# Performance work log

Measured on AMD Instinct MI355X. Metric: run time of the kernel, lower is better.

Reference implementation:

```python
import jax, jax.numpy as jnp
import numpy as np

B, S, VOCAB, HID, NH, L, SPAN = 4, 512, 25, 512, 8, 12, 512
HEAD = HID // NH
FF = 4 * HID
EPS = 1e-7  # DebertaV2 layer_norm_eps


def _ln(x, g, b):
    m = x.mean(-1, keepdims=True)
    v = ((x - m) ** 2).mean(-1, keepdims=True)
    return (x - m) / jnp.sqrt(v + EPS) * g + b


def setup_inputs() -> dict:
    key = jax.random.key(0)
    ks = iter(jax.random.split(key, 16))
    w = lambda shape: jax.random.normal(next(ks), shape, jnp.float32) * 0.05
    return {
        "x": jax.random.randint(next(ks), (B, S), 0, VOCAB),
        "attention_mask": jnp.ones((B, S), jnp.int32),
        "word_emb": w((VOCAB, HID)),
        "emb_ln_g": jnp.ones((HID,), jnp.float32),
        "emb_ln_b": jnp.zeros((HID,), jnp.float32),
        "rel_emb": w((2 * SPAN, HID)),
        "Wq": w((L, HID, HID)), "bq": jnp.zeros((L, HID), jnp.float32),
        "Wk": w((L, HID, HID)), "bk": jnp.zeros((L, HID), jnp.float32),
        "Wv": w((L, HID, HID)), "bv": jnp.zeros((L, HID), jnp.float32),
        "Wpk": w((L, HID, HID)), "bpk": jnp.zeros((L, HID), jnp.float32),
        "Wpq": w((L, HID, HID)), "bpq": jnp.zeros((L, HID), jnp.float32),
        "Wo": w((L, HID, HID)), "bo": jnp.zeros((L, HID), jnp.float32),
        "ln1_g": jnp.ones((L, HID), jnp.float32), "ln1_b": jnp.zeros((L, HID), jnp.float32),
        "W1": w((L, HID, FF)), "b1": jnp.zeros((L, FF), jnp.float32),
        "W2": w((L, FF, HID)), "b2": jnp.zeros((L, HID), jnp.float32),
        "ln2_g": jnp.ones((L, HID), jnp.float32), "ln2_b": jnp.zeros((L, HID), jnp.float32),
        "cls_w": w((VOCAB, HID)), "cls_b": jnp.zeros((VOCAB,), jnp.float32),
    }


def _forward(x, attention_mask, word_emb, emb_ln_g, emb_ln_b, rel_emb,
             Wq, bq, Wk, bk, Wv, bv, Wpk, bpk, Wpq, bpq, Wo, bo,
             ln1_g, ln1_b, W1, b1, W2, b2, ln2_g, ln2_b, cls_w, cls_b):
    mask = attention_mask.astype(jnp.float32)
    # embeddings: word only (position_biased_input=False), LN, then masked
    h = _ln(word_emb[x], emb_ln_g, emb_ln_b) * mask[..., None]

    rel = jnp.arange(S)[:, None] - jnp.arange(S)[None, :]          # q_pos - k_pos
    c2p_idx = jnp.clip(rel + SPAN, 0, 2 * SPAN - 1)[None, None]    # [1,1,S,S]
    p2c_idx = jnp.clip(-rel + SPAN, 0, 2 * SPAN - 1)[None, None]
    attm = (mask[:, None, None, :] * mask[:, None, :, None]) > 0   # [B,1,S,S]
    scale = jnp.sqrt(jnp.float32(HEAD * 3))                        # scale_factor = 1 + len(pos_att_type)
    neg = jnp.finfo(jnp.float32).min

    def heads(t):  # [B,S,HID] -> [B,NH,S,HEAD]
        return t.reshape(B, S, NH, HEAD).transpose(0, 2, 1, 3)

    for l in range(L):
        q = heads(h @ Wq[l] + bq[l])
        k = heads(h @ Wk[l] + bk[l])
        v = heads(h @ Wv[l] + bv[l])
        # projected relative-position embeddings: [NH, 2*SPAN, HEAD]
        pk = (rel_emb @ Wpk[l] + bpk[l]).reshape(2 * SPAN, NH, HEAD).transpose(1, 0, 2)
        pq = (rel_emb @ Wpq[l] + bpq[l]).reshape(2 * SPAN, NH, HEAD).transpose(1, 0, 2)

        scores = jnp.einsum('bhqd,bhkd->bhqk', q, k)
        # c2p: query content vs key position, gathered at clamp(rel+span)
        c2p = jnp.take_along_axis(jnp.einsum('bhqd,hpd->bhqp', q, pk), c2p_idx, axis=-1)
        # p2c: key content vs query position, gathered at clamp(-rel+span) then transposed
        p2c = jnp.take_along_axis(jnp.einsum('bhkd,hpd->bhkp', k, pq), p2c_idx, axis=-1)
        scores = (scores + c2p + jnp.swapaxes(p2c, -1, -2)) / scale

        scores = jnp.where(attm, scores, neg)
        probs = jnp.where(attm, jax.nn.softmax(scores, axis=-1), 0.0)  # XSoftmax
        ctx = jnp.einsum('bhqk,bhkd->bhqd', probs, v).transpose(0, 2, 1, 3).reshape(B, S, HID)
        h = _ln(ctx @ Wo[l] + bo[l] + h, ln1_g[l], ln1_b[l])
        f = jax.nn.gelu(h @ W1[l] + b1[l], approximate=False) @ W2[l] + b2[l]
        h = _ln(f + h, ln2_g[l], ln2_b[l])

    logits = h @ cls_w.T + cls_b
    return h, logits


def reference(x, attention_mask, word_emb, emb_ln_g, emb_ln_b, rel_emb,
              Wq, bq, Wk, bk, Wv, bv, Wpk, bpk, Wpq, bpq, Wo, bo,
              ln1_g, ln1_b, W1, b1, W2, b2, ln2_g, ln2_b, cls_w, cls_b):
    return _forward(x, attention_mask, word_emb, emb_ln_g, emb_ln_b, rel_emb,
                    Wq, bq, Wk, bk, Wv, bv, Wpk, bpk, Wpq, bpq, Wo, bo,
                    ln1_g, ln1_b, W1, b1, W2, b2, ln2_g, ln2_b, cls_w, cls_b)
```

## Files before the change

kernel.cpp:

```cpp
#include <hip/hip_runtime.h>
#include <hip/hip_bf16.h>

#define BATCH  4
#define SEQ    512
#define TOK    (BATCH*SEQ)
#define HID    512
#define NHEAD  8
#define HEAD   64
#define FFDIM  2048
#define NLAYER 12
#define SPAN2  1024
#define VOCAB  25
#define LNEPS  1e-7f
#define NEG_BIG -3.0e38f

typedef __attribute__((ext_vector_type(8))) short bf16x8;
typedef __attribute__((ext_vector_type(4))) float floatx4;

#define MFMA16(a, b, c) __builtin_amdgcn_mfma_f32_16x16x32_bf16((a), (b), (c), 0, 0, 0)

__device__ __forceinline__ float b2f(unsigned short u) {
    return __uint_as_float(((unsigned int)u) << 16);
}
__device__ __forceinline__ unsigned short f2b(float f) {
    __hip_bfloat16 h = __float2bfloat16(f);
    return *(unsigned short*)&h;
}

__device__ __forceinline__ float block_reduce_sum(float v, float* red) {
    int tid = threadIdx.x;
    red[tid] = v; __syncthreads();
    for (int s = 128; s > 0; s >>= 1) { if (tid < s) red[tid] += red[tid + s]; __syncthreads(); }
    float r = red[0]; __syncthreads();
    return r;
}

__global__ void embed_ln_kernel(const int* __restrict__ x, const int* __restrict__ am,
                                const float* __restrict__ word_emb,
                                const float* __restrict__ g, const float* __restrict__ bb,
                                float* __restrict__ h, unsigned short* __restrict__ hb) {
    __shared__ float red[256];
    int t = blockIdx.x, tid = threadIdx.x;
    const float* we = word_emb + (size_t)x[t] * HID;
    float v1 = we[tid], v2 = we[tid + 256];
    float mean = block_reduce_sum(v1 + v2, red) * (1.0f / HID);
    float d1 = v1 - mean, d2 = v2 - mean;
    float var = block_reduce_sum(d1 * d1 + d2 * d2, red) * (1.0f / HID);
    float rstd = rsqrtf(var + LNEPS);
    float maskf = (float)am[t];
    size_t base = (size_t)t * HID;
    float o1 = (d1 * rstd * g[tid]       + bb[tid])       * maskf;
    float o2 = (d2 * rstd * g[tid + 256] + bb[tid + 256]) * maskf;
    h[base + tid] = o1;        h[base + tid + 256] = o2;
    hb[base + tid] = f2b(o1);  hb[base + tid + 256] = f2b(o2);
}

__global__ void add_ln_kernel(const float* __restrict__ tmp,
                              const float* __restrict__ g, const float* __restrict__ bb,
                              float* __restrict__ h, unsigned short* __restrict__ hb) {
    __shared__ float red[256];
    int t = blockIdx.x, tid = threadIdx.x;
    size_t base = (size_t)t * HID;
    float v1 = tmp[base + tid] + h[base + tid];
    float v2 = tmp[base + tid + 256] + h[base + tid + 256];
    float mean = block_reduce_sum(v1 + v2, red) * (1.0f / HID);
    float d1 = v1 - mean, d2 = v2 - mean;
    float var = block_reduce_sum(d1 * d1 + d2 * d2, red) * (1.0f / HID);
    float rstd = rsqrtf(var + LNEPS);
    float o1 = d1 * rstd * g[tid]       + bb[tid];
    float o2 = d2 * rstd * g[tid + 256] + bb[tid + 256];
    h[base + tid] = o1;        h[base + tid + 256] = o2;
    hb[base + tid] = f2b(o1);  hb[base + tid + 256] = f2b(o2);
}

__global__ void add_ln2_kernel(const float* __restrict__ t1a, const float* __restrict__ t1b,
                               const float* __restrict__ g, const float* __restrict__ bb,
                               float* __restrict__ h, unsigned short* __restrict__ hb) {
    __shared__ float red[256];
    int t = blockIdx.x, tid = threadIdx.x;
    size_t base = (size_t)t * HID;
    float v1 = t1a[base + tid] + t1b[base + tid] + h[base + tid];
    float v2 = t1a[base + tid + 256] + t1b[base + tid + 256] + h[base + tid + 256];
    float mean = block_reduce_sum(v1 + v2, red) * (1.0f / HID);
    float d1 = v1 - mean, d2 = v2 - mean;
    float var = block_reduce_sum(d1 * d1 + d2 * d2, red) * (1.0f / HID);
    float rstd = rsqrtf(var + LNEPS);
    float o1 = d1 * rstd * g[tid]       + bb[tid];
    float o2 = d2 * rstd * g[tid + 256] + bb[tid + 256];
    h[base + tid] = o1;        h[base + tid + 256] = o2;
    hb[base + tid] = f2b(o1);  hb[base + tid + 256] = f2b(o2);
}

__global__ void cvt_rel_kernel(const float* __restrict__ in, unsigned short* __restrict__ out) {
    int i = (blockIdx.x * 256 + threadIdx.x) * 4;
    float4 v = *(const float4*)(in + i);
    out[i] = f2b(v.x); out[i+1] = f2b(v.y); out[i+2] = f2b(v.z); out[i+3] = f2b(v.w);
}

__global__ void tcvt_kernel(const float* __restrict__ in, unsigned short* __restrict__ out,
                            int K, int N) {
    __shared__ float tile[32][33];
    int l = blockIdx.z;
    const float* ip = in + (size_t)l * K * N;
    unsigned short* op = out + (size_t)l * K * N;
    int kb = blockIdx.y * 32, nb = blockIdx.x * 32;
    int tx = threadIdx.x, ty = threadIdx.y;
    #pragma unroll
    for (int i = 0; i < 32; i += 8) tile[ty + i][tx] = ip[(size_t)(kb + ty + i) * N + nb + tx];
    __syncthreads();
    #pragma unroll
    for (int i = 0; i < 32; i += 8) op[(size_t)(nb + ty + i) * K + kb + tx] = f2b(tile[tx][ty + i]);
}

__global__ void tcvt6_kernel(const float* __restrict__ Wq, const float* __restrict__ Wk,
                             const float* __restrict__ Wv, const float* __restrict__ Wpk,
                             const float* __restrict__ Wpq, const float* __restrict__ Wo,
                             unsigned short* __restrict__ out) {
    __shared__ float tile[32][33];
    int z = blockIdx.z, l = z / 6, w = z - l * 6;
    const float* src = w == 0 ? Wq : w == 1 ? Wk : w == 2 ? Wv : w == 3 ? Wpk : w == 4 ? Wpq : Wo;
    const float* ip = src + (size_t)l * HID * HID;
    unsigned short* op = out + ((size_t)w * NLAYER + l) * HID * HID;
    int kb = blockIdx.y * 32, nb = blockIdx.x * 32;
    int tx = threadIdx.x, ty = threadIdx.y;
    #pragma unroll
    for (int i = 0; i < 32; i += 8) tile[ty + i][tx] = ip[(size_t)(kb + ty + i) * HID + nb + tx];
    __syncthreads();
    #pragma unroll
    for (int i = 0; i < 32; i += 8) op[(size_t)(nb + ty + i) * HID + kb + tx] = f2b(tile[tx][ty + i]);
}

__device__ __forceinline__ void gemm_tile_bt(
    const unsigned short* __restrict__ A, const unsigned short* __restrict__ Bt,
    int row0, int col0, int K, int kbeg, int kend,
    floatx4 (&acc)[2][2], unsigned short (&As)[2][64][72], unsigned short (&Bs)[2][64][72]) {
    int tid = threadIdx.x;
    int lane = tid & 63, wid = tid >> 6;
    int wm = wid >> 1, wn = wid & 1;
    int m16 = lane & 15, quad = lane >> 4;
    int sr = tid >> 2, sc = (tid & 3) << 4;
    const unsigned short* Ag = A + (size_t)(row0 + sr) * K + sc;
    const unsigned short* Bg = Bt + (size_t)(col0 + sr) * K + sc;

    uint4 av0 = *(const uint4*)(Ag + kbeg);
    uint4 av1 = *(const uint4*)(Ag + kbeg + 8);
    uint4 bv0 = *(const uint4*)(Bg + kbeg);
    uint4 bv1 = *(const uint4*)(Bg + kbeg + 8);
    *(uint4*)&As[0][sr][sc]     = av0;
    *(uint4*)&As[0][sr][sc + 8] = av1;
    *(uint4*)&Bs[0][sr][sc]     = bv0;
    *(uint4*)&Bs[0][sr][sc + 8] = bv1;
    __syncthreads();

    int cur = 0;
    for (int k0 = kbeg; k0 < kend; k0 += 64) {
        int k1 = k0 + 64;
        bool more = k1 < kend;
        if (more) {
            av0 = *(const uint4*)(Ag + k1);
            av1 = *(const uint4*)(Ag + k1 + 8);
            bv0 = *(const uint4*)(Bg + k1);
            bv1 = *(const uint4*)(Bg + k1 + 8);
        }
        #pragma unroll
        for (int kk = 0; kk < 2; kk++) {
            bf16x8 a0 = *(const bf16x8*)&As[cur][wm * 32 + m16][kk * 32 + quad * 8];
            bf16x8 a1 = *(const bf16x8*)&As[cur][wm * 32 + 16 + m16][kk * 32 + quad * 8];
            bf16x8 b0 = *(const bf16x8*)&Bs[cur][wn * 32 + m16][kk * 32 + quad * 8];
            bf16x8 b1 = *(const bf16x8*)&Bs[cur][wn * 32 + 16 + m16][kk * 32 + quad * 8];
            acc[0][0] = MFMA16(a0, b0, acc[0][0]);
            acc[0][1] = MFMA16(a0, b1, acc[0][1]);
            acc[1][0] = MFMA16(a1, b0, acc[1][0]);
            acc[1][1] = MFMA16(a1, b1, acc[1][1]);
        }
        if (more) {
            *(uint4*)&As[cur ^ 1][sr][sc]     = av0;
            *(uint4*)&As[cur ^ 1][sr][sc + 8] = av1;
            *(uint4*)&Bs[cur ^ 1][sr][sc]     = bv0;
            *(uint4*)&Bs[cur ^ 1][sr][sc + 8] = bv1;
            __syncthreads();
            cur ^= 1;
        }
    }
}

template<bool OUT_BF16, bool GELU, int SPLITK>
__global__ __launch_bounds__(256) void gemm_bt(
    const unsigned short* __restrict__ A, const unsigned short* __restrict__ Bt,
    const float* __restrict__ bias, void* __restrict__ Cp, int N, int K) {
    __shared__ unsigned short As[2][64][72], Bs[2][64][72];
    int row0 = blockIdx.y * 64, col0 = blockIdx.x * 64;
    int kseg = K / SPLITK;
    int kbeg = kseg * blockIdx.z, kend = kbeg + kseg;
    floatx4 acc[2][2];
    #pragma unroll
    for (int mi = 0; mi < 2; mi++)
        #pragma unroll
        for (int ni = 0; ni < 2; ni++) acc[mi][ni] = (floatx4){0.f, 0.f, 0.f, 0.f};
    gemm_tile_bt(A, Bt, row0, col0, K, kbeg, kend, acc, As, Bs);

    int tid = threadIdx.x, lane = tid & 63, wid = tid >> 6;
    int wm = wid >> 1, wn = wid & 1, m16 = lane & 15, quad = lane >> 4;
    size_t outoff = (size_t)blockIdx.z * (size_t)(gridDim.y << 6) * N;
    #pragma unroll
    for (int ni = 0; ni < 2; ni++) {
        int colg = col0 + wn * 32 + ni * 16 + m16;
        float bval = (SPLITK == 1 || blockIdx.z == 0) ? bias[colg] : 0.0f;
        #pragma unroll
        for (int mi = 0; mi < 2; mi++) {
            #pragma unroll
            for (int r = 0; r < 4; r++) {
                int rowg = row0 + wm * 32 + mi * 16 + quad * 4 + r;
                float v = acc[mi][ni][r] + bval;
                if (GELU) v = 0.5f * v * (1.0f + erff(v * 0.70710678118654752f));
                if (OUT_BF16) ((unsigned short*)Cp)[(size_t)rowg * N + colg] = f2b(v);
                else          ((float*)Cp)[outoff + (size_t)rowg * N + colg] = v;
            }
        }
    }
}

__global__ __launch_bounds__(256) void qkvp_gemm(
    const unsigned short* __restrict__ hb, const unsigned short* __restrict__ relb,
    const unsigned short* __restrict__ Wqt, const unsigned short* __restrict__ Wkt,
    const unsigned short* __restrict__ Wvt, const unsigned short* __restrict__ Wpkt,
    const unsigned short* __restrict__ Wpqt,
    const float* __restrict__ bq, const float* __restrict__ bk, const float* __restrict__ bv,
    const float* __restrict__ bpk, const float* __restrict__ bpq,
    unsigned short* __restrict__ qb, unsigned short* __restrict__ kb,
    unsigned short* __restrict__ vb, unsigned short* __restrict__ pkb,
    unsigned short* __restrict__ pqb) {
    __shared__ unsigned short As[2][64][72], Bs[2][64][72];
    int bid = blockIdx.x;
    int xcd = bid & 7, slot = bid >> 3;
    int op, j;
    if (xcd < 6) { op = xcd >> 1; j = slot * 2 + (xcd & 1); }
    else         { op = xcd - 3;  j = slot; }
    int trow = j >> 3, tcol = j & 7;
    const unsigned short* A; const unsigned short* Bt; const float* bias; unsigned short* C;
    if (op < 3) {
        A = hb;
        Bt   = op == 0 ? Wqt : op == 1 ? Wkt : Wvt;
        bias = op == 0 ? bq  : op == 1 ? bk  : bv;
        C    = op == 0 ? qb  : op == 1 ? kb  : vb;
    } else {
        A = relb;
        Bt   = op == 3 ? Wpkt : Wpqt;
        bias = op == 3 ? bpk  : bpq;
        C    = op == 3 ? pkb  : pqb;
    }
    floatx4 acc[2][2];
    #pragma unroll
    for (int mi = 0; mi < 2; mi++)
        #pragma unroll
        for (int ni = 0; ni < 2; ni++) acc[mi][ni] = (floatx4){0.f, 0.f, 0.f, 0.f};
    gemm_tile_bt(A, Bt, trow * 64, tcol * 64, HID, 0, HID, acc, As, Bs);

    int tid = threadIdx.x, lane = tid & 63, wid = tid >> 6;
    int wm = wid >> 1, wn = wid & 1, m16 = lane & 15, quad = lane >> 4;
    #pragma unroll
    for (int ni = 0; ni < 2; ni++) {
        int colg = tcol * 64 + wn * 32 + ni * 16 + m16;
        float bval = bias[colg];
        #pragma unroll
        for (int mi = 0; mi < 2; mi++) {
            #pragma unroll
            for (int r = 0; r < 4; r++) {
                int rowg = trow * 64 + wm * 32 + mi * 16 + quad * 4 + r;
                C[(size_t)rowg * HID + colg] = f2b(acc[mi][ni][r] + bval);
            }
        }
    }
}

template<bool OUT_BF16, bool GELU>
__global__ __launch_bounds__(256) void mfma_gemm(
    const unsigned short* __restrict__ A, const float* __restrict__ B,
    const float* __restrict__ bias, void* __restrict__ Cp, int N, int K) {
    __shared__ unsigned short As[64][72];
    __shared__ unsigned short Bs[64][72];
    int tid = threadIdx.x;
    int lane = tid & 63, wid = tid >> 6;
    int wm = wid >> 1, wn = wid & 1;
    int row0 = blockIdx.y * 64, col0 = blockIdx.x * 64;
    int m16 = lane & 15, quad = lane >> 4;

    int ar = tid >> 2, ac = (tid & 3) << 4;
    int bk = (tid >> 3) << 1, bn = (tid & 7) << 3;

    const unsigned short* Ag = A + (size_t)(row0 + ar) * K + ac;
    const float* Bg = B + (size_t)bk * N + col0 + bn;

    floatx4 acc[2][2];
    #pragma unroll
    for (int mi = 0; mi < 2; mi++)
        #pragma unroll
        for (int ni = 0; ni < 2; ni++) acc[mi][ni] = (floatx4){0.f, 0.f, 0.f, 0.f};

    for (int k0 = 0; k0 < K; k0 += 64) {
        uint4 av0 = *(const uint4*)(Ag + k0);
        uint4 av1 = *(const uint4*)(Ag + k0 + 8);
        const float* br0 = Bg + (size_t)k0 * N;
        const float* br1 = br0 + N;
        float4 b00 = *(const float4*)br0, b01 = *(const float4*)(br0 + 4);
        float4 b10 = *(const float4*)br1, b11 = *(const float4*)(br1 + 4);
        *(uint4*)&As[ar][ac] = av0;
        *(uint4*)&As[ar][ac + 8] = av1;
        float lo[8] = {b00.x, b00.y, b00.z, b00.w, b01.x, b01.y, b01.z, b01.w};
        float hi[8] = {b10.x, b10.y, b10.z, b10.w, b11.x, b11.y, b11.z, b11.w};
        #pragma unroll
        for (int i = 0; i < 8; i++) {
            unsigned int p = (unsigned int)f2b(lo[i]) | ((unsigned int)f2b(hi[i]) << 16);
            *(unsigned int*)&Bs[bn + i][bk] = p;
        }
        __syncthreads();
        #pragma unroll
        for (int kk = 0; kk < 2; kk++) {
            bf16x8 a0 = *(const bf16x8*)&As[wm * 32 + m16][kk * 32 + quad * 8];
            bf16x8 a1 = *(const bf16x8*)&As[wm * 32 + 16 + m16][kk * 32 + quad * 8];
            bf16x8 b0 = *(const bf16x8*)&Bs[wn * 32 + m16][kk * 32 + quad * 8];
            bf16x8 b1 = *(const bf16x8*)&Bs[wn * 32 + 16 + m16][kk * 32 + quad * 8];
            acc[0][0] = MFMA16(a0, b0, acc[0][0]);
            acc[0][1] = MFMA16(a0, b1, acc[0][1]);
            acc[1][0] = MFMA16(a1, b0, acc[1][0]);
            acc[1][1] = MFMA16(a1, b1, acc[1][1]);
        }
        __syncthreads();
    }
    #pragma unroll
    for (int ni = 0; ni < 2; ni++) {
        int colg = col0 + wn * 32 + ni * 16 + m16;
        float bv = bias[colg];
        #pragma unroll
        for (int mi = 0; mi < 2; mi++) {
            #pragma unroll
            for (int r = 0; r < 4; r++) {
                int rowg = row0 + wm * 32 + mi * 16 + quad * 4 + r;
                float v = acc[mi][ni][r] + bv;
                if (GELU) v = 0.5f * v * (1.0f + erff(v * 0.70710678118654752f));
                if (OUT_BF16) ((unsigned short*)Cp)[(size_t)rowg * N + colg] = f2b(v);
                else          ((float*)Cp)[(size_t)rowg * N + colg] = v;
            }
        }
    }
}

__global__ __launch_bounds__(256, 2) void attn_kernel(
    const unsigned short* __restrict__ Q, const unsigned short* __restrict__ K,
    const unsigned short* __restrict__ V,
    const unsigned short* __restrict__ PK, const unsigned short* __restrict__ PQ,
    const int* __restrict__ am, unsigned short* __restrict__ ctx) {
    __shared__ unsigned short Ks[2][32][72];
    __shared__ unsigned short Vt[2][64][40];
    __shared__ float Afs[4][16][49];
    __shared__ float Bfs[4][32][50];
    __shared__ unsigned short Pls[4][16][40];
    __shared__ int mkk[2][32];
    __shared__ float mergeML[2][2][16];

    int bid = blockIdx.x;
    int hh = bid & 7;
    int b  = (bid >> 3) & 3;
    int q0 = (bid >> 5) * 32;
    int tid = threadIdx.x;
    int lane = tid & 63, wave = tid >> 6;
    int u = wave >> 1;
    int s = wave & 1;
    int quad = lane >> 4, m16 = lane & 15;
    const float inv_scale = 0.07216878364870323f;

    const unsigned short* qg = Q + (size_t)(b * SEQ + q0 + u * 16 + m16) * HID + hh * HEAD;
    bf16x8 qf0 = *(const bf16x8*)(qg + quad * 8);
    bf16x8 qf1 = *(const bf16x8*)(qg + 32 + quad * 8);

    int sr = tid >> 3;
    int sc = (tid & 7) * 8;
    int vkey = ((sc >> 3) & 3) << 3;

    floatx4 accO[4];
    #pragma unroll
    for (int nt = 0; nt < 4; nt++) accO[nt] = (floatx4){0.f, 0.f, 0.f, 0.f};
    float mreg[4] = {NEG_BIG, NEG_BIG, NEG_BIG, NEG_BIG};
    float lreg[4] = {0.f, 0.f, 0.f, 0.f};

    for (int ph = 0; ph < 8; ph++) {
        int t = 2 * ph + s;
        int P0  = q0 - 32 * t + 481;
        int P20 = 32 * t - q0 + 481;
        int Jb  = 16 - 16 * u;

        bf16x8 pkf[3][2], pqf[3][2];
        #pragma unroll
        for (int nt = 0; nt < 3; nt++) {
            int prow = P0 + 16 * u + nt * 16 + m16;
            const unsigned short* pg = PK + (size_t)prow * HID + hh * HEAD + quad * 8;
            pkf[nt][0] = *(const bf16x8*)pg;
            pkf[nt][1] = *(const bf16x8*)(pg + 32);
            int prow2 = P20 + Jb + nt * 16 + m16;
            if (prow2 > 1023) prow2 = 1023;
            const unsigned short* pg2 = PQ + (size_t)prow2 * HID + hh * HEAD + quad * 8;
            pqf[nt][0] = *(const bf16x8*)pg2;
            pqf[nt][1] = *(const bf16x8*)(pg2 + 32);
        }

        #pragma unroll
        for (int sl = 0; sl < 2; sl++) {
            int k0 = ph * 64 + sl * 32;
            const unsigned short* kg = K + (size_t)(b * SEQ + k0 + sr) * HID + hh * HEAD + sc;
            *(uint4*)&Ks[sl][sr][sc] = *(const uint4*)kg;
            uint4 vv = *(const uint4*)(V + (size_t)(b * SEQ + k0 + sr) * HID + hh * HEAD + sc);
            unsigned short* vp = (unsigned short*)&vv;
            #pragma unroll
            for (int j = 0; j < 8; j++) Vt[sl][sc + j][sr ^ vkey] = vp[j];
        }
        if (tid < 64) mkk[tid >> 5][tid & 31] = am[b * SEQ + ph * 64 + tid];
        __syncthreads();

        floatx4 accS[2];
        accS[0] = (floatx4){0.f, 0.f, 0.f, 0.f};
        accS[1] = (floatx4){0.f, 0.f, 0.f, 0.f};
        #pragma unroll
        for (int n = 0; n < 2; n++) {
            bf16x8 kfa = *(const bf16x8*)&Ks[s][n * 16 + m16][quad * 8];
            bf16x8 kfb = *(const bf16x8*)&Ks[s][n * 16 + m16][32 + quad * 8];
            accS[n] = MFMA16(qf0, kfa, accS[n]);
            accS[n] = MFMA16(qf1, kfb, accS[n]);
        }

        {
            floatx4 accA[3];
            #pragma unroll
            for (int nt = 0; nt < 3; nt++) {
                accA[nt] = (floatx4){0.f, 0.f, 0.f, 0.f};
                accA[nt] = MFMA16(qf0, pkf[nt][0], accA[nt]);
                accA[nt] = MFMA16(qf1, pkf[nt][1], accA[nt]);
            }
            #pragma unroll
            for (int nt = 0; nt < 3; nt++)
                #pragma unroll
                for (int r = 0; r < 4; r++)
                    Afs[wave][quad * 4 + r][nt * 16 + m16] = accA[nt][r];
        }

        {
            floatx4 accB[2][3];
            #pragma unroll
            for (int mt = 0; mt < 2; mt++) {
                bf16x8 afa = *(const bf16x8*)&Ks[s][mt * 16 + m16][quad * 8];
                bf16x8 afb = *(const bf16x8*)&Ks[s][mt * 16 + m16][32 + quad * 8];
                #pragma unroll
                for (int nt = 0; nt < 3; nt++) {
                    accB[mt][nt] = (floatx4){0.f, 0.f, 0.f, 0.f};
                    accB[mt][nt] = MFMA16(afa, pqf[nt][0], accB[mt][nt]);
                    accB[mt][nt] = MFMA16(afb, pqf[nt][1], accB[mt][nt]);
                }
            }
            #pragma unroll
            for (int mt = 0; mt < 2; mt++)
                #pragma unroll
                for (int nt = 0; nt < 3; nt++)
                    #pragma unroll
                    for (int r = 0; r < 4; r++)
                        Bfs[wave][mt * 16 + quad * 4 + r][nt * 16 + m16] = accB[mt][nt][r];
        }

        float sv[2][4];
        float tmax[4] = {NEG_BIG, NEG_BIG, NEG_BIG, NEG_BIG};
        #pragma unroll
        for (int n = 0; n < 2; n++) {
            #pragma unroll
            for (int r = 0; r < 4; r++) {
                int qq = quad * 4 + r;
                int kc = n * 16 + m16;
                float av = Afs[wave][qq][qq - kc + 31];
                float bv = Bfs[wave][kc][kc - qq + 15];
                float x = (accS[n][r] + av + bv) * inv_scale;
                x = mkk[s][kc] ? x : NEG_BIG;
                sv[n][r] = x;
                tmax[r] = fmaxf(tmax[r], x);
            }
        }
        float alpha[4], psum[4];
        #pragma unroll
        for (int r = 0; r < 4; r++) {
            float tm = tmax[r];
            tm = fmaxf(tm, __shfl_xor(tm, 1));
            tm = fmaxf(tm, __shfl_xor(tm, 2));
            tm = fmaxf(tm, __shfl_xor(tm, 4));
            tm = fmaxf(tm, __shfl_xor(tm, 8));
            float mo = mreg[r];
            float mn = fmaxf(mo, tm);
            alpha[r] = __expf(mo - mn);
            mreg[r] = mn;
        }
        #pragma unroll
        for (int r = 0; r < 4; r++) psum[r] = 0.f;
        #pragma unroll
        for (int n = 0; n < 2; n++) {
            #pragma unroll
            for (int r = 0; r < 4; r++) {
                float p = (sv[n][r] > -1.5e38f) ? __expf(sv[n][r] - mreg[r]) : 0.0f;
                unsigned short pb = f2b(p);
                Pls[wave][quad * 4 + r][n * 16 + m16] = pb;
                psum[r] += b2f(pb);
            }
        }
        #pragma unroll
        for (int r = 0; r < 4; r++) {
            float ps = psum[r];
            ps += __shfl_xor(ps, 1);
            ps += __shfl_xor(ps, 2);
            ps += __shfl_xor(ps, 4);
            ps += __shfl_xor(ps, 8);
            lreg[r] = lreg[r] * alpha[r] + ps;
        }
        #pragma unroll
        for (int nt = 0; nt < 4; nt++)
            #pragma unroll
            for (int r = 0; r < 4; r++) accO[nt][r] *= alpha[r];
        {
            bf16x8 pf = *(const bf16x8*)&Pls[wave][m16][quad * 8];
            #pragma unroll
            for (int nt = 0; nt < 4; nt++) {
                int d = nt * 16 + m16;
                int kq = (quad ^ ((d >> 3) & 3)) * 8;
                bf16x8 vf = *(const bf16x8*)&Vt[s][d][kq];
                accO[nt] = MFMA16(pf, vf, accO[nt]);
            }
        }
        __syncthreads();
    }

    __syncthreads();
    float* mo = &Bfs[0][0][0];
    if (s == 1) {
        #pragma unroll
        for (int nt = 0; nt < 4; nt++)
            #pragma unroll
            for (int r = 0; r < 4; r++)
                mo[u * 1056 + (quad * 4 + r) * 66 + nt * 16 + m16] = accO[nt][r];
        if (m16 == 0) {
            #pragma unroll
            for (int r = 0; r < 4; r++) {
                mergeML[u][0][quad * 4 + r] = mreg[r];
                mergeML[u][1][quad * 4 + r] = lreg[r];
            }
        }
    }
    __syncthreads();
    if (s == 0) {
        #pragma unroll
        for (int r = 0; r < 4; r++) {
            int row = quad * 4 + r;
            float m1 = mergeML[u][0][row], l1 = mergeML[u][1][row];
            float m0 = mreg[r], l0 = lreg[r];
            float mt = fmaxf(m0, m1);
            float a0 = __expf(m0 - mt), a1 = __expf(m1 - mt);
            float lt = l0 * a0 + l1 * a1;
            float inv = lt > 0.0f ? 1.0f / lt : 0.0f;
            inv *= (float)am[b * SEQ + q0 + u * 16 + row];
            #pragma unroll
            for (int nt = 0; nt < 4; nt++) {
                float o1 = mo[u * 1056 + row * 66 + nt * 16 + m16];
                float val = (accO[nt][r] * a0 + o1 * a1) * inv;
                ctx[(size_t)(b * SEQ + q0 + u * 16 + row) * HID + hh * HEAD + nt * 16 + m16] = f2b(val);
            }
        }
    }
}

__global__ void copy_f_kernel(const float* __restrict__ in, float* __restrict__ out, int n) {
    int i = blockIdx.x * 256 + threadIdx.x;
    if (i < n) out[i] = in[i];
}
__global__ void cls_kernel(const float* __restrict__ h, const float* __restrict__ cls_w,
                           const float* __restrict__ cls_b, float* __restrict__ out) {
    int t = blockIdx.x, v = threadIdx.x;
    if (v < VOCAB) {
        const float* hr = h + (size_t)t * HID;
        const float* wr = cls_w + (size_t)v * HID;
        float acc = cls_b[v];
        for (int d = 0; d < HID; d++) acc += hr[d] * wr[d];
        out[t * VOCAB + v] = acc;
    }
}

extern "C" void kernel_launch(void* const* d_in, const int* in_sizes, int n_in,
                              void* d_out, int out_size, void* d_ws, size_t ws_size,
                              hipStream_t stream) {
    const int* x     = (const int*)d_in[0];
    const int* am    = (const int*)d_in[1];
    const float* word_emb = (const float*)d_in[2];
    const float* emb_g    = (const float*)d_in[3];
    const float* emb_b    = (const float*)d_in[4];
    const float* rel_emb  = (const float*)d_in[5];
    const float* Wq  = (const float*)d_in[6];  const float* bq  = (const float*)d_in[7];
    const float* Wk  = (const float*)d_in[8];  const float* bk  = (const float*)d_in[9];
    const float* Wv  = (const float*)d_in[10]; const float* bv  = (const float*)d_in[11];
    const float* Wpk = (const float*)d_in[12]; const float* bpk = (const float*)d_in[13];
    const float* Wpq = (const float*)d_in[14]; const float* bpq = (const float*)d_in[15];
    const float* Wo  = (const float*)d_in[16]; const float* bo  = (const float*)d_in[17];
    const float* ln1g = (const float*)d_in[18]; const float* ln1b = (const float*)d_in[19];
    const float* W1  = (const float*)d_in[20]; const float* b1  = (const float*)d_in[21];
    const float* W2  = (const float*)d_in[22]; const float* b2  = (const float*)d_in[23];
    const float* ln2g = (const float*)d_in[24]; const float* ln2b = (const float*)d_in[25];
    const float* cls_w = (const float*)d_in[26]; const float* cls_b = (const float*)d_in[27];

    char* wsb = (char*)d_ws;
    const size_t NEED_BIG = 107u << 20;

    if (ws_size >= NEED_BIG) {
        float* h  = (float*)wsb;
        float* t1 = (float*)(wsb + (4u << 20));
        float* t2 = (float*)(wsb + (8u << 20));
        unsigned short* qb   = (unsigned short*)(wsb + (12u << 20));
        unsigned short* kb   = (unsigned short*)(wsb + (14u << 20));
        unsigned short* vb   = (unsigned short*)(wsb + (16u << 20));
        unsigned short* pkb  = (unsigned short*)(wsb + (18u << 20));
        unsigned short* pqb  = (unsigned short*)(wsb + (19u << 20));
        unsigned short* relb = (unsigned short*)(wsb + (20u << 20));
        unsigned short* hb   = (unsigned short*)(wsb + (21u << 20));
        unsigned short* ctx  = hb;
        unsigned short* ffb  = qb;
        unsigned short* Wqt  = (unsigned short*)(wsb + (23u << 20));
        unsigned short* W1t  = (unsigned short*)(wsb + (59u << 20));
        unsigned short* W2t  = (unsigned short*)(wsb + (83u << 20));

        const size_t M512 = (size_t)HID * HID;

        tcvt6_kernel<<<dim3(16, 16, 72), dim3(32, 8), 0, stream>>>(Wq, Wk, Wv, Wpk, Wpq, Wo, Wqt);
        tcvt_kernel<<<dim3(64, 16, 12), dim3(32, 8), 0, stream>>>(W1, W1t, HID, FFDIM);
        tcvt_kernel<<<dim3(16, 64, 12), dim3(32, 8), 0, stream>>>(W2, W2t, FFDIM, HID);
        cvt_rel_kernel<<<dim3(SPAN2 * HID / 1024), dim3(256), 0, stream>>>(rel_emb, relb);
        embed_ln_kernel<<<dim3(TOK), dim3(256), 0, stream>>>(x, am, word_emb, emb_g, emb_b, h, hb);

        for (int l = 0; l < NLAYER; l++) {
            qkvp_gemm<<<dim3(1024), dim3(256), 0, stream>>>(
                hb, relb,
                Wqt + (size_t)(0 * NLAYER + l) * M512, Wqt + (size_t)(1 * NLAYER + l) * M512,
                Wqt + (size_t)(2 * NLAYER + l) * M512, Wqt + (size_t)(3 * NLAYER + l) * M512,
                Wqt + (size_t)(4 * NLAYER + l) * M512,
                bq + l * HID, bk + l * HID, bv + l * HID, bpk + l * HID, bpq + l * HID,
                qb, kb, vb, pkb, pqb);

            attn_kernel<<<dim3(512), dim3(256), 0, stream>>>(
                qb, kb, vb, pkb, pqb, am, ctx);

            gemm_bt<false, false, 2><<<dim3(HID / 64, TOK / 64, 2), dim3(256), 0, stream>>>(
                ctx, Wqt + (size_t)(5 * NLAYER + l) * M512, bo + l * HID, t1, HID, HID);
            add_ln2_kernel<<<dim3(TOK), dim3(256), 0, stream>>>(t1, t2, ln1g + l * HID, ln1b + l * HID, h, hb);

            gemm_bt<true, true, 1><<<dim3(FFDIM / 64, TOK / 64, 1), dim3(256), 0, stream>>>(
                hb, W1t + (size_t)l * HID * FFDIM, b1 + l * FFDIM, ffb, FFDIM, HID);
            gemm_bt<false, false, 2><<<dim3(HID / 64, TOK / 64, 2), dim3(256), 0, stream>>>(
                ffb, W2t + (size_t)l * HID * FFDIM, b2 + l * HID, t1, HID, FFDIM);
            add_ln2_kernel<<<dim3(TOK), dim3(256), 0, stream>>>(t1, t2, ln2g + l * HID, ln2b + l * HID, h, hb);
        }

        float* out_f = (float*)d_out;
        copy_f_kernel<<<dim3(TOK * HID / 256), dim3(256), 0, stream>>>(h, out_f, TOK * HID);
        cls_kernel<<<dim3(TOK), dim3(32), 0, stream>>>(h, cls_w, cls_b, out_f + TOK * HID);
        return;
    }

    const size_t NEEDED = 19u << 20;
    if (ws_size < NEEDED) return;
    float* h  = (float*)wsb;
    float* t1 = (float*)(wsb + (4u << 20));
    unsigned short* qb   = (unsigned short*)(wsb + (8u << 20));
    unsigned short* kb   = qb  + (1u << 20);
    unsigned short* vb   = kb  + (1u << 20);
    unsigned short* pkb  = vb  + (1u << 20);
    unsigned short* pqb  = pkb + (1u << 19);
    unsigned short* relb = (unsigned short*)(wsb + (16u << 20));
    unsigned short* hb   = (unsigned short*)(wsb + (17u << 20));
    unsigned short* ctx  = hb;
    unsigned short* ffb  = qb;

    cvt_rel_kernel<<<dim3(SPAN2 * HID / 1024), dim3(256), 0, stream>>>(rel_emb, relb);
    embed_ln_kernel<<<dim3(TOK), dim3(256), 0, stream>>>(x, am, word_emb, emb_g, emb_b, h, hb);

    for (int l = 0; l < NLAYER; l++) {
        const float* Wq_l = Wq + (size_t)l * HID * HID;
        const float* Wk_l = Wk + (size_t)l * HID * HID;
        const float* Wv_l = Wv + (size_t)l * HID * HID;
        const float* Wo_l = Wo + (size_t)l * HID * HID;
        const float* Wpk_l = Wpk + (size_t)l * HID * HID;
        const float* Wpq_l = Wpq + (size_t)l * HID * HID;
        const float* W1_l = W1 + (size_t)l * HID * FFDIM;
        const float* W2_l = W2 + (size_t)l * FFDIM * HID;

        mfma_gemm<true,  false><<<dim3(HID/64, TOK/64),   dim3(256), 0, stream>>>(hb,   Wq_l,  bq + l*HID,  qb,  HID, HID);
        mfma_gemm<true,  false><<<dim3(HID/64, TOK/64),   dim3(256), 0, stream>>>(hb,   Wk_l,  bk + l*HID,  kb,  HID, HID);
        mfma_gemm<true,  false><<<dim3(HID/64, TOK/64),   dim3(256), 0, stream>>>(hb,   Wv_l,  bv + l*HID,  vb,  HID, HID);
        mfma_gemm<true,  false><<<dim3(HID/64, SPAN2/64), dim3(256), 0, stream>>>(relb, Wpk_l, bpk + l*HID, pkb, HID, HID);
        mfma_gemm<true,  false><<<dim3(HID/64, SPAN2/64), dim3(256), 0, stream>>>(relb, Wpq_l, bpq + l*HID, pqb, HID, HID);

        attn_kernel<<<dim3(512), dim3(256), 0, stream>>>(qb, kb, vb, pkb, pqb, am, ctx);

        mfma_gemm<false, false><<<dim3(HID/64, TOK/64),   dim3(256), 0, stream>>>(ctx,  Wo_l,  bo + l*HID,  t1,  HID, HID);
        add_ln_kernel<<<dim3(TOK), dim3(256), 0, stream>>>(t1, ln1g + l*HID, ln1b + l*HID, h, hb);

        mfma_gemm<true,  true ><<<dim3(FFDIM/64, TOK/64), dim3(256), 0, stream>>>(hb,   W1_l,  b1 + l*FFDIM, ffb, FFDIM, HID);
        mfma_gemm<false, false><<<dim3(HID/64, TOK/64),   dim3(256), 0, stream>>>(ffb,  W2_l,  b2 + l*HID,  t1,  HID, FFDIM);
        add_ln_kernel<<<dim3(TOK), dim3(256), 0, stream>>>(t1, ln2g + l*HID, ln2b + l*HID, h, hb);
    }

    float* out_f = (float*)d_out;
    copy_f_kernel<<<dim3(TOK*HID/256), dim3(256), 0, stream>>>(h, out_f, TOK*HID);
    cls_kernel<<<dim3(TOK), dim3(32), 0, stream>>>(h, cls_w, cls_b, out_f + TOK*HID);
}
```

Baseline: 1.431 ms.

## Enlarge GEMM tiles to 128 rows, use wave-per-row LayerNorm, prefetch attention PQ

GEMM kernels move from 64x64 to 128x64 block tiles, with four M sub-tiles per wave that reuse each B fragment, and launch bounds request two blocks per CU. The LayerNorm kernels switch to one wavefront per token, using shuffle reductions and vectorized float4 loads and stores instead of shared-memory block reductions. The attention kernel double-buffers the position-key and position-query fragment loads so the next phase's loads are issued before the current phase's compute. Larger tiles halve the grid size, which may reduce parallelism on a many-CU GPU, and they raise register pressure.

New measurement: 1.424 ms. Within noise of the previous version (-0.5%).

```diff
diff --git a/kernel.cpp b/kernel.cpp
--- a/kernel.cpp
+++ b/kernel.cpp
@@ -27,68 +27,79 @@
     return *(unsigned short*)&h;
 }
 
-__device__ __forceinline__ float block_reduce_sum(float v, float* red) {
-    int tid = threadIdx.x;
-    red[tid] = v; __syncthreads();
-    for (int s = 128; s > 0; s >>= 1) { if (tid < s) red[tid] += red[tid + s]; __syncthreads(); }
-    float r = red[0]; __syncthreads();
-    return r;
+__device__ __forceinline__ float wave_sum(float v) {
+    #pragma unroll
+    for (int o = 1; o < 64; o <<= 1) v += __shfl_xor(v, o);
+    return v;
+}
+
+__device__ __forceinline__ void ln_finish(const float (&v)[8], const float* __restrict__ g,
+                                          const float* __restrict__ bb, int lane, float maskf,
+                                          size_t base, float* __restrict__ h,
+                                          unsigned short* __restrict__ hb) {
+    float sum = 0.f;
+    #pragma unroll
+    for (int j = 0; j < 8; j++) sum += v[j];
+    float mean = wave_sum(sum) * (1.0f / HID);
+    float d[8]; float var = 0.f;
+    #pragma unroll
+    for (int j = 0; j < 8; j++) { d[j] = v[j] - mean; var += d[j] * d[j]; }
+    float rstd = rsqrtf(wave_sum(var) * (1.0f / HID) + LNEPS);
+    const float* gp = g + lane * 8; const float* bp = bb + lane * 8;
+    float4 g0 = *(const float4*)gp, g1 = *(const float4*)(gp + 4);
+    float4 b0 = *(const float4*)bp, b1 = *(const float4*)(bp + 4);
+    float gg[8] = {g0.x, g0.y, g0.z, g0.w, g1.x, g1.y, g1.z, g1.w};
+    float bv[8] = {b0.x, b0.y, b0.z, b0.w, b1.x, b1.y, b1.z, b1.w};
+    float o8[8];
+    #pragma unroll
+    for (int j = 0; j < 8; j++) o8[j] = (d[j] * rstd * gg[j] + bv[j]) * maskf;
+    *(float4*)(h + base)     = make_float4(o8[0], o8[1], o8[2], o8[3]);
+    *(float4*)(h + base + 4) = make_float4(o8[4], o8[5], o8[6], o8[7]);
+    uint4 pb;
+    pb.x = (unsigned int)f2b(o8[0]) | ((unsigned int)f2b(o8[1]) << 16);
+    pb.y = (unsigned int)f2b(o8[2]) | ((unsigned int)f2b(o8[3]) << 16);
+    pb.z = (unsigned int)f2b(o8[4]) | ((unsigned int)f2b(o8[5]) << 16);
+    pb.w = (unsigned int)f2b(o8[6]) | ((unsigned int)f2b(o8[7]) << 16);
+    *(uint4*)(hb + base) = pb;
 }
 
 __global__ void embed_ln_kernel(const int* __restrict__ x, const int* __restrict__ am,
                                 const float* __restrict__ word_emb,
                                 const float* __restrict__ g, const float* __restrict__ bb,
                                 float* __restrict__ h, unsigned short* __restrict__ hb) {
-    __shared__ float red[256];
-    int t = blockIdx.x, tid = threadIdx.x;
-    const float* we = word_emb + (size_t)x[t] * HID;
-    float v1 = we[tid], v2 = we[tid + 256];
-    float mean = block_reduce_sum(v1 + v2, red) * (1.0f / HID);
-    float d1 = v1 - mean, d2 = v2 - mean;
-    float var = block_reduce_sum(d1 * d1 + d2 * d2, red) * (1.0f / HID);
-    float rstd = rsqrtf(var + LNEPS);
-    float maskf = (float)am[t];
-    size_t base = (size_t)t * HID;
-    float o1 = (d1 * rstd * g[tid]       + bb[tid])       * maskf;
-    float o2 = (d2 * rstd * g[tid + 256] + bb[tid + 256]) * maskf;
-    h[base + tid] = o1;        h[base + tid + 256] = o2;
-    hb[base + tid] = f2b(o1);  hb[base + tid + 256] = f2b(o2);
+    int wv = threadIdx.x >> 6, lane = threadIdx.x & 63;
+    int t = blockIdx.x * 4 + wv;
+    const float* we = word_emb + (size_t)x[t] * HID + lane * 8;
+    float4 va = *(const float4*)we, vb2 = *(const float4*)(we + 4);
+    float v[8] = {va.x, va.y, va.z, va.w, vb2.x, vb2.y, vb2.z, vb2.w};
+    ln_finish(v, g, bb, lane, (float)am[t], (size_t)t * HID + lane * 8, h, hb);
 }
 
 __global__ void add_ln_kernel(const float* __restrict__ tmp,
                               const float* __restrict__ g, const float* __restrict__ bb,
                               float* __restrict__ h, unsigned short* __restrict__ hb) {
-    __shared__ float red[256];
-    int t = blockIdx.x, tid = threadIdx.x;
-    size_t base = (size_t)t * HID;
-    float v1 = tmp[base + tid] + h[base + tid];
-    float v2 = tmp[base + tid + 256] + h[base + tid + 256];
-    float mean = block_reduce_sum(v1 + v2, red) * (1.0f / HID);
-    float d1 = v1 - mean, d2 = v2 - mean;
-    float var = block_reduce_sum(d1 * d1 + d2 * d2, red) * (1.0f / HID);
-    float rstd = rsqrtf(var + LNEPS);
-    float o1 = d1 * rstd * g[tid]       + bb[tid];
-    float o2 = d2 * rstd * g[tid + 256] + bb[tid + 256];
-    h[base + tid] = o1;        h[base + tid + 256] = o2;
-    hb[base + tid] = f2b(o1);  hb[base + tid + 256] = f2b(o2);
+    int wv = threadIdx.x >> 6, lane = threadIdx.x & 63;
+    int t = blockIdx.x * 4 + wv;
+    size_t base = (size_t)t * HID + lane * 8;
+    float4 ta = *(const float4*)(tmp + base), tb = *(const float4*)(tmp + base + 4);
+    float4 ha = *(const float4*)(h + base),  hbb = *(const float4*)(h + base + 4);
+    float v[8] = {ta.x + ha.x, ta.y + ha.y, ta.z + ha.z, ta.w + ha.w,
+                  tb.x + hbb.x, tb.y + hbb.y, tb.z + hbb.z, tb.w + hbb.w};
+    ln_finish(v, g, bb, lane, 1.0f, base, h, hb);
 }
 
 __global__ void add_ln2_kernel(const float* __restrict__ t1a, const float* __restrict__ t1b,
                                const float* __restrict__ g, const float* __restrict__ bb,
                                float* __restrict__ h, unsigned short* __restrict__ hb) {
-    __shared__ float red[256];
-    int t = blockIdx.x, tid = threadIdx.x;
-    size_t base = (size_t)t * HID;
-    float v1 = t1a[base + tid] + t1b[base + tid] + h[base + tid];
-    float v2 = t1a[base + tid + 256] + t1b[base + tid + 256] + h[base + tid + 256];
-    float mean = block_reduce_sum(v1 + v2, red) * (1.0f / HID);
-    float d1 = v1 - mean, d2 = v2 - mean;
-    float var = block_reduce_sum(d1 * d1 + d2 * d2, red) * (1.0f / HID);
-    float rstd = rsqrtf(var + LNEPS);
-    float o1 = d1 * rstd * g[tid]       + bb[tid];
-    float o2 = d2 * rstd * g[tid + 256] + bb[tid + 256];
-    h[base + tid] = o1;        h[base + tid + 256] = o2;
-    hb[base + tid] = f2b(o1);  hb[base + tid + 256] = f2b(o2);
+    int wv = threadIdx.x >> 6, lane = threadIdx.x & 63;
+    int t = blockIdx.x * 4 + wv;
+    size_t base = (size_t)t * HID + lane * 8;
+    float4 aa = *(const float4*)(t1a + base), ab = *(const float4*)(t1a + base + 4);
+    float4 ba = *(const float4*)(t1b + base), bbv = *(const float4*)(t1b + base + 4);
+    float4 ha = *(const float4*)(h + base),  hb2 = *(const float4*)(h + base + 4);
+    float v[8] = {aa.x + ba.x + ha.x, aa.y + ba.y + ha.y, aa.z + ba.z + ha.z, aa.w + ba.w + ha.w,
+                  ab.x + bbv.x + hb2.x, ab.y + bbv.y + hb2.y, ab.z + bbv.z + hb2.z, ab.w + bbv.w + hb2.w};
+    ln_finish(v, g, bb, lane, 1.0f, base, h, hb);
 }
 
 __global__ void cvt_rel_kernel(const float* __restrict__ in, unsigned short* __restrict__ out) {
@@ -130,26 +141,28 @@
     for (int i = 0; i < 32; i += 8) op[(size_t)(nb + ty + i) * HID + kb + tx] = f2b(tile[tx][ty + i]);
 }
 
-__device__ __forceinline__ void gemm_tile_bt(
+__device__ __forceinline__ void gemm_core128(
     const unsigned short* __restrict__ A, const unsigned short* __restrict__ Bt,
     int row0, int col0, int K, int kbeg, int kend,
-    floatx4 (&acc)[2][2], unsigned short (&As)[2][64][72], unsigned short (&Bs)[2][64][72]) {
+    floatx4 (&acc)[4][2], unsigned short (&As)[2][128][72], unsigned short (&Bs)[2][64][72]) {
     int tid = threadIdx.x;
     int lane = tid & 63, wid = tid >> 6;
     int wm = wid >> 1, wn = wid & 1;
     int m16 = lane & 15, quad = lane >> 4;
-    int sr = tid >> 2, sc = (tid & 3) << 4;
-    const unsigned short* Ag = A + (size_t)(row0 + sr) * K + sc;
-    const unsigned short* Bg = Bt + (size_t)(col0 + sr) * K + sc;
-
-    uint4 av0 = *(const uint4*)(Ag + kbeg);
-    uint4 av1 = *(const uint4*)(Ag + kbeg + 8);
-    uint4 bv0 = *(const uint4*)(Bg + kbeg);
-    uint4 bv1 = *(const uint4*)(Bg + kbeg + 8);
-    *(uint4*)&As[0][sr][sc]     = av0;
-    *(uint4*)&As[0][sr][sc + 8] = av1;
-    *(uint4*)&Bs[0][sr][sc]     = bv0;
-    *(uint4*)&Bs[0][sr][sc + 8] = bv1;
+    int asr = tid >> 1, asc = (tid & 1) * 32;
+    int bsr = tid >> 2, bsc = (tid & 3) * 16;
+    const unsigned short* Ag = A + (size_t)(row0 + asr) * K + asc;
+    const unsigned short* Bg = Bt + (size_t)(col0 + bsr) * K + bsc;
+
+    uint4 a0 = *(const uint4*)(Ag + kbeg),      a1 = *(const uint4*)(Ag + kbeg + 8);
+    uint4 a2 = *(const uint4*)(Ag + kbeg + 16), a3 = *(const uint4*)(Ag + kbeg + 24);
+    uint4 b0 = *(const uint4*)(Bg + kbeg),      b1 = *(const uint4*)(Bg + kbeg + 8);
+    *(uint4*)&As[0][asr][asc]      = a0;
+    *(uint4*)&As[0][asr][asc + 8]  = a1;
+    *(uint4*)&As[0][asr][asc + 16] = a2;
+    *(uint4*)&As[0][asr][asc + 24] = a3;
+    *(uint4*)&Bs[0][bsr][bsc]      = b0;
+    *(uint4*)&Bs[0][bsr][bsc + 8]  = b1;
     __syncthreads();
 
     int cur = 0;
@@ -157,27 +170,28 @@
         int k1 = k0 + 64;
         bool more = k1 < kend;
         if (more) {
-            av0 = *(const uint4*)(Ag + k1);
-            av1 = *(const uint4*)(Ag + k1 + 8);
-            bv0 = *(const uint4*)(Bg + k1);
-            bv1 = *(const uint4*)(Bg + k1 + 8);
+            a0 = *(const uint4*)(Ag + k1);      a1 = *(const uint4*)(Ag + k1 + 8);
+            a2 = *(const uint4*)(Ag + k1 + 16); a3 = *(const uint4*)(Ag + k1 + 24);
+            b0 = *(const uint4*)(Bg + k1);      b1 = *(const uint4*)(Bg + k1 + 8);
         }
         #pragma unroll
         for (int kk = 0; kk < 2; kk++) {
-            bf16x8 a0 = *(const bf16x8*)&As[cur][wm * 32 + m16][kk * 32 + quad * 8];
-            bf16x8 a1 = *(const bf16x8*)&As[cur][wm * 32 + 16 + m16][kk * 32 + quad * 8];
-            bf16x8 b0 = *(const bf16x8*)&Bs[cur][wn * 32 + m16][kk * 32 + quad * 8];
-            bf16x8 b1 = *(const bf16x8*)&Bs[cur][wn * 32 + 16 + m16][kk * 32 + quad * 8];
-            acc[0][0] = MFMA16(a0, b0, acc[0][0]);
-            acc[0][1] = MFMA16(a0, b1, acc[0][1]);
-            acc[1][0] = MFMA16(a1, b0, acc[1][0]);
-            acc[1][1] = MFMA16(a1, b1, acc[1][1]);
+            bf16x8 bf0 = *(const bf16x8*)&Bs[cur][wn * 32 + m16][kk * 32 + quad * 8];
+            bf16x8 bf1 = *(const bf16x8*)&Bs[cur][wn * 32 + 16 + m16][kk * 32 + quad * 8];
+            #pragma unroll
+            for (int mi = 0; mi < 4; mi++) {
+                bf16x8 af = *(const bf16x8*)&As[cur][wm * 64 + mi * 16 + m16][kk * 32 + quad * 8];
+                acc[mi][0] = MFMA16(af, bf0, acc[mi][0]);
+                acc[mi][1] = MFMA16(af, bf1, acc[mi][1]);
+            }
         }
         if (more) {
-            *(uint4*)&As[cur ^ 1][sr][sc]     = av0;
-            *(uint4*)&As[cur ^ 1][sr][sc + 8] = av1;
-            *(uint4*)&Bs[cur ^ 1][sr][sc]     = bv0;
-            *(uint4*)&Bs[cur ^ 1][sr][sc + 8] = bv1;
+            *(uint4*)&As[cur ^ 1][asr][asc]      = a0;
+            *(uint4*)&As[cur ^ 1][asr][asc + 8]  = a1;
+            *(uint4*)&As[cur ^ 1][asr][asc + 16] = a2;
+            *(uint4*)&As[cur ^ 1][asr][asc + 24] = a3;
+            *(uint4*)&Bs[cur ^ 1][bsr][bsc]      = b0;
+            *(uint4*)&Bs[cur ^ 1][bsr][bsc + 8]  = b1;
             __syncthreads();
             cur ^= 1;
         }
@@ -185,32 +199,32 @@
 }
 
 template<bool OUT_BF16, bool GELU, int SPLITK>
-__global__ __launch_bounds__(256) void gemm_bt(
+__global__ __launch_bounds__(256, 2) void gemm_bt2(
     const unsigned short* __restrict__ A, const unsigned short* __restrict__ Bt,
     const float* __restrict__ bias, void* __restrict__ Cp, int N, int K) {
-    __shared__ unsigned short As[2][64][72], Bs[2][64][72];
-    int row0 = blockIdx.y * 64, col0 = blockIdx.x * 64;
+    __shared__ unsigned short As[2][128][72], Bs[2][64][72];
+    int row0 = blockIdx.y * 128, col0 = blockIdx.x * 64;
     int kseg = K / SPLITK;
     int kbeg = kseg * blockIdx.z, kend = kbeg + kseg;
-    floatx4 acc[2][2];
-    #pragma unroll
-    for (int mi = 0; mi < 2; mi++)
+    floatx4 acc[4][2];
+    #pragma unroll
+    for (int mi = 0; mi < 4; mi++)
         #pragma unroll
         for (int ni = 0; ni < 2; ni++) acc[mi][ni] = (floatx4){0.f, 0.f, 0.f, 0.f};
-    gemm_tile_bt(A, Bt, row0, col0, K, kbeg, kend, acc, As, Bs);
+    gemm_core128(A, Bt, row0, col0, K, kbeg, kend, acc, As, Bs);
 
     int tid = threadIdx.x, lane = tid & 63, wid = tid >> 6;
     int wm = wid >> 1, wn = wid & 1, m16 = lane & 15, quad = lane >> 4;
-    size_t outoff = (size_t)blockIdx.z * (size_t)(gridDim.y << 6) * N;
+    size_t outoff = (size_t)blockIdx.z * (size_t)(gridDim.y << 7) * N;
     #pragma unroll
     for (int ni = 0; ni < 2; ni++) {
         int colg = col0 + wn * 32 + ni * 16 + m16;
         float bval = (SPLITK == 1 || blockIdx.z == 0) ? bias[colg] : 0.0f;
         #pragma unroll
-        for (int mi = 0; mi < 2; mi++) {
+        for (int mi = 0; mi < 4; mi++) {
             #pragma unroll
             for (int r = 0; r < 4; r++) {
-                int rowg = row0 + wm * 32 + mi * 16 + quad * 4 + r;
+                int rowg = row0 + wm * 64 + mi * 16 + quad * 4 + r;
                 float v = acc[mi][ni][r] + bval;
                 if (GELU) v = 0.5f * v * (1.0f + erff(v * 0.70710678118654752f));
                 if (OUT_BF16) ((unsigned short*)Cp)[(size_t)rowg * N + colg] = f2b(v);
@@ -220,7 +234,7 @@
     }
 }
 
-__global__ __launch_bounds__(256) void qkvp_gemm(
+__global__ __launch_bounds__(256, 2) void qkvp_gemm(
     const unsigned short* __restrict__ hb, const unsigned short* __restrict__ relb,
     const unsigned short* __restrict__ Wqt, const unsigned short* __restrict__ Wkt,
     const unsigned short* __restrict__ Wvt, const unsigned short* __restrict__ Wpkt,
@@ -230,7 +244,7 @@
     unsigned short* __restrict__ qb, unsigned short* __restrict__ kb,
     unsigned short* __restrict__ vb, unsigned short* __restrict__ pkb,
     unsigned short* __restrict__ pqb) {
-    __shared__ unsigned short As[2][64][72], Bs[2][64][72];
+    __shared__ unsigned short As[2][128][72], Bs[2][64][72];
     int bid = blockIdx.x;
     int xcd = bid & 7, slot = bid >> 3;
     int op, j;
@@ -249,12 +263,12 @@
         bias = op == 3 ? bpk  : bpq;
         C    = op == 3 ? pkb  : pqb;
     }
-    floatx4 acc[2][2];
-    #pragma unroll
-    for (int mi = 0; mi < 2; mi++)
+    floatx4 acc[4][2];
+    #pragma unroll
+    for (int mi = 0; mi < 4; mi++)
         #pragma unroll
         for (int ni = 0; ni < 2; ni++) acc[mi][ni] = (floatx4){0.f, 0.f, 0.f, 0.f};
-    gemm_tile_bt(A, Bt, trow * 64, tcol * 64, HID, 0, HID, acc, As, Bs);
+    gemm_core128(A, Bt, trow * 128, tcol * 64, HID, 0, HID, acc, As, Bs);
 
     int tid = threadIdx.x, lane = tid & 63, wid = tid >> 6;
     int wm = wid >> 1, wn = wid & 1, m16 = lane & 15, quad = lane >> 4;
@@ -263,10 +277,10 @@
         int colg = tcol * 64 + wn * 32 + ni * 16 + m16;
         float bval = bias[colg];
         #pragma unroll
-        for (int mi = 0; mi < 2; mi++) {
+        for (int mi = 0; mi < 4; mi++) {
             #pragma unroll
             for (int r = 0; r < 4; r++) {
-                int rowg = trow * 64 + wm * 32 + mi * 16 + quad * 4 + r;
+                int rowg = trow * 128 + wm * 64 + mi * 16 + quad * 4 + r;
                 C[(size_t)rowg * HID + colg] = f2b(acc[mi][ni][r] + bval);
             }
         }
@@ -383,13 +397,10 @@
     float mreg[4] = {NEG_BIG, NEG_BIG, NEG_BIG, NEG_BIG};
     float lreg[4] = {0.f, 0.f, 0.f, 0.f};
 
-    for (int ph = 0; ph < 8; ph++) {
-        int t = 2 * ph + s;
+    auto loadPQ = [&](int t, bf16x8 (&pkf)[3][2], bf16x8 (&pqf)[3][2]) {
         int P0  = q0 - 32 * t + 481;
         int P20 = 32 * t - q0 + 481;
         int Jb  = 16 - 16 * u;
-
-        bf16x8 pkf[3][2], pqf[3][2];
         #pragma unroll
         for (int nt = 0; nt < 3; nt++) {
             int prow = P0 + 16 * u + nt * 16 + m16;
@@ -402,7 +413,9 @@
             pqf[nt][0] = *(const bf16x8*)pg2;
             pqf[nt][1] = *(const bf16x8*)(pg2 + 32);
         }
-
+    };
+
+    auto stageKV = [&](int ph) {
         #pragma unroll
         for (int sl = 0; sl < 2; sl++) {
             int k0 = ph * 64 + sl * 32;
@@ -414,8 +427,9 @@
             for (int j = 0; j < 8; j++) Vt[sl][sc + j][sr ^ vkey] = vp[j];
         }
         if (tid < 64) mkk[tid >> 5][tid & 31] = am[b * SEQ + ph * 64 + tid];
-        __syncthreads();
-
+    };
+
+    auto computePhase = [&](bf16x8 (&pkf)[3][2], bf16x8 (&pqf)[3][2]) {
         floatx4 accS[2];
         accS[0] = (floatx4){0.f, 0.f, 0.f, 0.f};
         accS[1] = (floatx4){0.f, 0.f, 0.f, 0.f};
@@ -426,7 +440,6 @@
             accS[n] = MFMA16(qf0, kfa, accS[n]);
             accS[n] = MFMA16(qf1, kfb, accS[n]);
         }
-
         {
             floatx4 accA[3];
             #pragma unroll
@@ -441,7 +454,6 @@
                 for (int r = 0; r < 4; r++)
                     Afs[wave][quad * 4 + r][nt * 16 + m16] = accA[nt][r];
         }
-
         {
             floatx4 accB[2][3];
             #pragma unroll
@@ -463,7 +475,6 @@
                     for (int r = 0; r < 4; r++)
                         Bfs[wave][mt * 16 + quad * 4 + r][nt * 16 + m16] = accB[mt][nt][r];
         }
-
         float sv[2][4];
         float tmax[4] = {NEG_BIG, NEG_BIG, NEG_BIG, NEG_BIG};
         #pragma unroll
@@ -528,7 +539,28 @@
                 accO[nt] = MFMA16(pf, vf, accO[nt]);
             }
         }
-        __syncthreads();
+    };
+
+    bf16x8 pkfA[3][2], pqfA[3][2], pkfB[3][2], pqfB[3][2];
+    loadPQ(s, pkfA, pqfA);
+    #pragma unroll
+    for (int pp = 0; pp < 4; pp++) {
+        {
+            int ph = 2 * pp;
+            __syncthreads();
+            stageKV(ph);
+            __syncthreads();
+            if (ph < 7) loadPQ(2 * (ph + 1) + s, pkfB, pqfB);
+            computePhase(pkfA, pqfA);
+        }
+        {
+            int ph = 2 * pp + 1;
+            __syncthreads();
+            stageKV(ph);
+            __syncthreads();
+            if (ph < 7) loadPQ(2 * (ph + 1) + s, pkfA, pqfA);
+            computePhase(pkfB, pqfB);
+        }
     }
 
     __syncthreads();
@@ -632,10 +664,10 @@
         tcvt_kernel<<<dim3(64, 16, 12), dim3(32, 8), 0, stream>>>(W1, W1t, HID, FFDIM);
         tcvt_kernel<<<dim3(16, 64, 12), dim3(32, 8), 0, stream>>>(W2, W2t, FFDIM, HID);
         cvt_rel_kernel<<<dim3(SPAN2 * HID / 1024), dim3(256), 0, stream>>>(rel_emb, relb);
-        embed_ln_kernel<<<dim3(TOK), dim3(256), 0, stream>>>(x, am, word_emb, emb_g, emb_b, h, hb);
+        embed_ln_kernel<<<dim3(TOK / 4), dim3(256), 0, stream>>>(x, am, word_emb, emb_g, emb_b, h, hb);
 
         for (int l = 0; l < NLAYER; l++) {
-            qkvp_gemm<<<dim3(1024), dim3(256), 0, stream>>>(
+            qkvp_gemm<<<dim3(512), dim3(256), 0, stream>>>(
                 hb, relb,
                 Wqt + (size_t)(0 * NLAYER + l) * M512, Wqt + (size_t)(1 * NLAYER + l) * M512,
                 Wqt + (size_t)(2 * NLAYER + l) * M512, Wqt + (size_t)(3 * NLAYER + l) * M512,
@@ -646,15 +678,15 @@
             attn_kernel<<<dim3(512), dim3(256), 0, stream>>>(
                 qb, kb, vb, pkb, pqb, am, ctx);
 
-            gemm_bt<false, false, 2><<<dim3(HID / 64, TOK / 64, 2), dim3(256), 0, stream>>>(
+            gemm_bt2<false, false, 2><<<dim3(HID / 64, TOK / 128, 2), dim3(256), 0, stream>>>(
                 ctx, Wqt + (size_t)(5 * NLAYER + l) * M512, bo + l * HID, t1, HID, HID);
-            add_ln2_kernel<<<dim3(TOK), dim3(256), 0, stream>>>(t1, t2, ln1g + l * HID, ln1b + l * HID, h, hb);
-
-            gemm_bt<true, true, 1><<<dim3(FFDIM / 64, TOK / 64, 1), dim3(256), 0, stream>>>(
+            add_ln2_kernel<<<dim3(TOK / 4), dim3(256), 0, stream>>>(t1, t2, ln1g + l * HID, ln1b + l * HID, h, hb);
+
+            gemm_bt2<true, true, 1><<<dim3(FFDIM / 64, TOK / 128, 1), dim3(256), 0, stream>>>(
                 hb, W1t + (size_t)l * HID * FFDIM, b1 + l * FFDIM, ffb, FFDIM, HID);
-            gemm_bt<false, false, 2><<<dim3(HID / 64, TOK / 64, 2), dim3(256), 0, stream>>>(
+            gemm_bt2<false, false, 2><<<dim3(HID / 64, TOK / 128, 2), dim3(256), 0, stream>>>(
                 ffb, W2t + (size_t)l * HID * FFDIM, b2 + l * HID, t1, HID, FFDIM);
-            add_ln2_kernel<<<dim3(TOK), dim3(256), 0, stream>>>(t1, t2, ln2g + l * HID, ln2b + l * HID, h, hb);
+            add_ln2_kernel<<<dim3(TOK / 4), dim3(256), 0, stream>>>(t1, t2, ln2g + l * HID, ln2b + l * HID, h, hb);
         }
 
         float* out_f = (float*)d_out;
@@ -678,7 +710,7 @@
     unsigned short* ffb  = qb;
 
     cvt_rel_kernel<<<dim3(SPAN2 * HID / 1024), dim3(256), 0, stream>>>(rel_emb, relb);
-    embed_ln_kernel<<<dim3(TOK), dim3(256), 0, stream>>>(x, am, word_emb, emb_g, emb_b, h, hb);
+    embed_ln_kernel<<<dim3(TOK / 4), dim3(256), 0, stream>>>(x, am, word_emb, emb_g, emb_b, h, hb);
 
     for (int l = 0; l < NLAYER; l++) {
         const float* Wq_l = Wq + (size_t)l * HID * HID;
@@ -699,11 +731,11 @@
         attn_kernel<<<dim3(512), dim3(256), 0, stream>>>(qb, kb, vb, pkb, pqb, am, ctx);
 
         mfma_gemm<false, false><<<dim3(HID/64, TOK/64),   dim3(256), 0, stream>>>(ctx,  Wo_l,  bo + l*HID,  t1,  HID, HID);
-        add_ln_kernel<<<dim3(TOK), dim3(256), 0, stream>>>(t1, ln1g + l*HID, ln1b + l*HID, h, hb);
+        add_ln_kernel<<<dim3(TOK / 4), dim3(256), 0, stream>>>(t1, ln1g + l*HID, ln1b + l*HID, h, hb);
 
         mfma_gemm<true,  true ><<<dim3(FFDIM/64, TOK/64), dim3(256), 0, stream>>>(hb,   W1_l,  b1 + l*FFDIM, ffb, FFDIM, HID);
         mfma_gemm<false, false><<<dim3(HID/64, TOK/64),   dim3(256), 0, stream>>>(ffb,  W2_l,  b2 + l*HID,  t1,  HID, FFDIM);
-        add_ln_kernel<<<dim3(TOK), dim3(256), 0, stream>>>(t1, ln2g + l*HID, ln2b + l*HID, h, hb);
+        add_ln_kernel<<<dim3(TOK / 4), dim3(256), 0, stream>>>(t1, ln2g + l*HID, ln2b + l*HID, h, hb);
     }
 
     float* out_f = (float*)d_out;
```
